# Performance work log

Hardware: AMD Instinct MI355X
Metric: run time of the kernel (lower is better)

Reference implementation:

```python
import jax, jax.numpy as jnp
import numpy as np

B, D_EMB, D_HID, D_FEAT = 16384, 128, 1024, 4096


def setup_inputs() -> dict:
    key = jax.random.key(0)
    ks = jax.random.split(key, 7)
    s = 0.05  # keep pre-sigmoid logits in a reasonable range
    return {
        "flat_emb": jax.random.normal(ks[0], (B, D_FEAT), dtype=jnp.float32),
        "fs1_ctx_bias": jax.random.normal(ks[1], (1, D_EMB), dtype=jnp.float32),
        "fs2_ctx_bias": jax.random.normal(ks[2], (1, D_EMB), dtype=jnp.float32),
        "fs1_W1": jax.random.normal(ks[3], (D_EMB, D_HID), dtype=jnp.float32) * s,
        "fs1_b1": jnp.zeros((D_HID,), dtype=jnp.float32),
        "fs1_W2": jax.random.normal(ks[4], (D_HID, D_FEAT), dtype=jnp.float32) * s,
        "fs1_b2": jnp.zeros((D_FEAT,), dtype=jnp.float32),
        "fs2_W1": jax.random.normal(ks[5], (D_EMB, D_HID), dtype=jnp.float32) * s,
        "fs2_b1": jnp.zeros((D_HID,), dtype=jnp.float32),
        "fs2_W2": jax.random.normal(ks[6], (D_HID, D_FEAT), dtype=jnp.float32) * s,
        "fs2_b2": jnpp_zeros((D_FEAT,)) if False else jnp.zeros((D_FEAT,), dtype=jnp.float32),
    }


def _gate(ctx_bias, W1, b1, W2, b2):
    # DNN: Linear -> ReLU -> Linear -> sigmoid. ctx_bias is [1, D_EMB];
    # the torch code repeats it over the batch, which is mathematically a
    # broadcast — compute the gate once and broadcast-multiply.
    h = jax.nn.relu(ctx_bias @ W1 + b1)            # [1, D_HID]
    return jax.nn.sigmoid(h @ W2 + b2) * 2.0        # [1, D_FEAT]


def reference(flat_emb, fs1_ctx_bias, fs2_ctx_bias,
              fs1_W1, fs1_b1, fs1_W2, fs1_b2,
              fs2_W1, fs2_b1, fs2_W2, fs2_b2):
    gt1 = _gate(fs1_ctx_bias, fs1_W1, fs1_b1, fs1_W2, fs1_b2)
    gt2 = _gate(fs2_ctx_bias, fs2_W1, fs2_b1, fs2_W2, fs2_b2)
    feature1 = flat_emb * gt1   # [B, D_FEAT]
    feature2 = flat_emb * gt2   # [B, D_FEAT]
    return (feature1, feature2)
```

## Files before the change

### kernel.cpp

```cpp
#include <hip/hip_runtime.h>
#include <math.h>

#define B_SZ   16384
#define D_EMB  128
#define D_HID  1024
#define D_FEAT 4096

__global__ __launch_bounds__(256) void gate_kernel(
    const float* __restrict__ ctx1, const float* __restrict__ ctx2,
    const float* __restrict__ W1a,  const float* __restrict__ b1a,
    const float* __restrict__ W2a,  const float* __restrict__ b2a,
    const float* __restrict__ W1b,  const float* __restrict__ b1b,
    const float* __restrict__ W2b,  const float* __restrict__ b2b,
    float* __restrict__ gates )
{
    const int blocks_per_gate = D_FEAT / 256;
    const int g   = blockIdx.x / blocks_per_gate;
    const int blk = blockIdx.x % blocks_per_gate;

    const float* ctx = (g == 0) ? ctx1 : ctx2;
    const float* W1  = (g == 0) ? W1a  : W1b;
    const float* b1  = (g == 0) ? b1a  : b1b;
    const float* W2  = (g == 0) ? W2a  : W2b;
    const float* b2  = (g == 0) ? b2a  : b2b;

    __shared__ float s_ctx[D_EMB];
    __shared__ float s_h[D_HID];

    const int t = threadIdx.x;
    if (t < D_EMB) s_ctx[t] = ctx[t];
    __syncthreads();

#pragma unroll
    for (int r = 0; r < D_HID / 256; ++r) {
        const int m = t + 256 * r;
        float acc = b1[m];
#pragma unroll 8
        for (int i = 0; i < D_EMB; ++i)
            acc = fmaf(s_ctx[i], W1[i * D_HID + m], acc);
        s_h[m] = acc > 0.0f ? acc : 0.0f;
    }
    __syncthreads();

    const int j = blk * 256 + t;
    float acc = b2[j];
#pragma unroll 8
    for (int k = 0; k < D_HID; ++k)
        acc = fmaf(s_h[k], W2[k * D_FEAT + j], acc);

    const float gval = 2.0f / (1.0f + expf(-acc));
    gates[g * D_FEAT + j] = gval;
}

__global__ __launch_bounds__(256) void mul_kernel(
    const float4* __restrict__ emb,
    const float4* __restrict__ gates,
    float4* __restrict__ out1,
    float4* __restrict__ out2)
{
    const int idx = blockIdx.x * blockDim.x + threadIdx.x;
    const int total = B_SZ * D_FEAT / 4;
    if (idx >= total) return;

    const int jg = idx & (D_FEAT / 4 - 1);

    const float4 e  = emb[idx];
    const float4 g1 = gates[jg];
    const float4 g2 = gates[D_FEAT / 4 + jg];

    float4 o1, o2;
    o1.x = e.x * g1.x; o1.y = e.y * g1.y; o1.z = e.z * g1.z; o1.w = e.w * g1.w;
    o2.x = e.x * g2.x; o2.y = e.y * g2.y; o2.z = e.z * g2.z; o2.w = e.w * g2.w;

    out1[idx] = o1;
    out2[idx] = o2;
}

extern "C" void kernel_launch(void* const* d_in, const int* in_sizes, int n_in,
                              void* d_out, int out_size, void* d_ws, size_t ws_size,
                              hipStream_t stream)
{
    const float* flat_emb = (const float*)d_in[0];
    const float* ctx1     = (const float*)d_in[1];
    const float* ctx2     = (const float*)d_in[2];
    const float* W1a      = (const float*)d_in[3];
    const float* b1a      = (const float*)d_in[4];
    const float* W2a      = (const float*)d_in[5];
    const float* b2a      = (const float*)d_in[6];
    const float* W1b      = (const float*)d_in[7];
    const float* b1b      = (const float*)d_in[8];
    const float* W2b      = (const float*)d_in[9];
    const float* b2b      = (const float*)d_in[10];

    float* out1  = (float*)d_out;
    float* out2  = (float*)d_out + (size_t)B_SZ * D_FEAT;
    float* gates = (float*)d_ws;

    gate_kernel<<<2 * (D_FEAT / 256), 256, 0, stream>>>(
        ctx1, ctx2, W1a, b1a, W2a, b2a, W1b, b1b, W2b, b2b, gates);

    const int total4 = B_SZ * D_FEAT / 4;
    mul_kernel<<<total4 / 256, 256, 0, stream>>>(
        (const float4*)flat_emb, (const float4*)gates,
        (float4*)out1, (float4*)out2);
}
```

Baseline: 813.3 us.

## Split gate MLP into two kernels with split-K, and make the multiply kernel grid-stride with nontemporal accesses

The hidden layer is now computed once per gate in its own small kernel. Before, each of the 32 gate blocks recomputed the full hidden vector. The second layer uses 256 blocks that split the K dimension 8 ways and reduce the partial sums in shared memory, which gives far more parallelism than the old 32-block launch. The multiply kernel now runs a fixed 2048-block grid in which each thread loops over rows, loads its gate values once, and uses nontemporal loads and stores for the streaming data. The cost is one extra kernel launch and a workspace round trip for the hidden vector.

```diff
diff --git a/kernel.cpp b/kernel.cpp
--- a/kernel.cpp
+++ b/kernel.cpp
@@ -6,74 +6,98 @@
 #define D_HID  1024
 #define D_FEAT 4096
 
-__global__ __launch_bounds__(256) void gate_kernel(
+typedef float f4 __attribute__((ext_vector_type(4)));
+
+__global__ __launch_bounds__(256) void h_kernel(
     const float* __restrict__ ctx1, const float* __restrict__ ctx2,
     const float* __restrict__ W1a,  const float* __restrict__ b1a,
-    const float* __restrict__ W2a,  const float* __restrict__ b2a,
     const float* __restrict__ W1b,  const float* __restrict__ b1b,
-    const float* __restrict__ W2b,  const float* __restrict__ b2b,
-    float* __restrict__ gates )
+    float* __restrict__ h )
 {
-    const int blocks_per_gate = D_FEAT / 256;
-    const int g   = blockIdx.x / blocks_per_gate;
-    const int blk = blockIdx.x % blocks_per_gate;
-
-    const float* ctx = (g == 0) ? ctx1 : ctx2;
-    const float* W1  = (g == 0) ? W1a  : W1b;
-    const float* b1  = (g == 0) ? b1a  : b1b;
-    const float* W2  = (g == 0) ? W2a  : W2b;
-    const float* b2  = (g == 0) ? b2a  : b2b;
+    const int g   = blockIdx.x >> 2;
+    const int blk = blockIdx.x & 3;
+    const float* ctx = g ? ctx2 : ctx1;
+    const float* W1  = g ? W1b  : W1a;
+    const float* b1  = g ? b1b  : b1a;
 
     __shared__ float s_ctx[D_EMB];
-    __shared__ float s_h[D_HID];
-
     const int t = threadIdx.x;
     if (t < D_EMB) s_ctx[t] = ctx[t];
     __syncthreads();
 
+    const int m = blk * 256 + t;
+    float acc = b1[m];
+#pragma unroll 8
+    for (int i = 0; i < D_EMB; ++i)
+        acc = fmaf(s_ctx[i], W1[i * D_HID + m], acc);
+    h[g * D_HID + m] = acc > 0.0f ? acc : 0.0f;
+}
+
+__global__ __launch_bounds__(256) void gate_kernel(
+    const float* __restrict__ W2a, const float* __restrict__ b2a,
+    const float* __restrict__ W2b, const float* __restrict__ b2b,
+    const float* __restrict__ h,
+    float* __restrict__ gates       )
+{
+    const int g   = blockIdx.x >> 7;
+    const int blk = blockIdx.x & 127;
+    const float* W2 = g ? W2b : W2a;
+    const float* b2 = g ? b2b : b2a;
+
+    __shared__ float s_h[D_HID];
+    __shared__ float s_part[256];
+
+    const int t = threadIdx.x;
 #pragma unroll
-    for (int r = 0; r < D_HID / 256; ++r) {
-        const int m = t + 256 * r;
-        float acc = b1[m];
-#pragma unroll 8
-        for (int i = 0; i < D_EMB; ++i)
-            acc = fmaf(s_ctx[i], W1[i * D_HID + m], acc);
-        s_h[m] = acc > 0.0f ? acc : 0.0f;
-    }
+    for (int r = 0; r < D_HID / 256; ++r)
+        s_h[t + 256 * r] = h[g * D_HID + t + 256 * r];
     __syncthreads();
 
-    const int j = blk * 256 + t;
-    float acc = b2[j];
+    const int tj = t & 31;
+    const int tk = t >> 5;
+    const int j  = blk * 32 + tj;
+
+    const float* w = W2 + (size_t)(tk * 128) * D_FEAT + j;
+    float p = 0.0f;
 #pragma unroll 8
-    for (int k = 0; k < D_HID; ++k)
-        acc = fmaf(s_h[k], W2[k * D_FEAT + j], acc);
+    for (int kk = 0; kk < 128; ++kk)
+        p = fmaf(s_h[tk * 128 + kk], w[(size_t)kk * D_FEAT], p);
 
-    const float gval = 2.0f / (1.0f + expf(-acc));
-    gates[g * D_FEAT + j] = gval;
+    s_part[tj * 8 + tk] = p;
+    __syncthreads();
+
+    if (t < 32) {
+        float a = b2[blk * 32 + t];
+#pragma unroll
+        for (int u = 0; u < 8; ++u) a += s_part[t * 8 + u];
+        gates[g * D_FEAT + blk * 32 + t] = 2.0f / (1.0f + expf(-a));
+    }
 }
 
 __global__ __launch_bounds__(256) void mul_kernel(
-    const float4* __restrict__ emb,
-    const float4* __restrict__ gates,
-    float4* __restrict__ out1,
-    float4* __restrict__ out2)
+    const f4* __restrict__ emb,
+    const f4* __restrict__ gates,
+    f4* __restrict__ out1,
+    f4* __restrict__ out2)
 {
-    const int idx = blockIdx.x * blockDim.x + threadIdx.x;
-    const int total = B_SZ * D_FEAT / 4;
-    if (idx >= total) return;
+    const int tid = blockIdx.x * 256 + threadIdx.x;
+    const int c   = tid & (D_FEAT / 4 - 1);
+    const int r0  = tid >> 10;
 
-    const int jg = idx & (D_FEAT / 4 - 1);
+    const f4 g1 = gates[c];
+    const f4 g2 = gates[D_FEAT / 4 + c];
 
-    const float4 e  = emb[idx];
-    const float4 g1 = gates[jg];
-    const float4 g2 = gates[D_FEAT / 4 + jg];
+    size_t idx = (size_t)r0 * (D_FEAT / 4) + c;
+    const size_t step = (size_t)512 * (D_FEAT / 4);
 
-    float4 o1, o2;
-    o1.x = e.x * g1.x; o1.y = e.y * g1.y; o1.z = e.z * g1.z; o1.w = e.w * g1.w;
-    o2.x = e.x * g2.x; o2.y = e.y * g2.y; o2.z = e.z * g2.z; o2.w = e.w * g2.w;
-
-    out1[idx] = o1;
-    out2[idx] = o2;
+#pragma unroll 4
+    for (int r = 0; r < B_SZ / 512; ++r, idx += step) {
+        f4 e  = __builtin_nontemporal_load(emb + idx);
+        f4 o1 = e * g1;
+        f4 o2 = e * g2;
+        __builtin_nontemporal_store(o1, out1 + idx);
+        __builtin_nontemporal_store(o2, out2 + idx);
+    }
 }
 
 extern "C" void kernel_launch(void* const* d_in, const int* in_sizes, int n_in,
@@ -95,12 +119,12 @@
     float* out1  = (float*)d_out;
     float* out2  = (float*)d_out + (size_t)B_SZ * D_FEAT;
     float* gates = (float*)d_ws;
+    float* h     = (float*)d_ws + 2 * D_FEAT;
 
-    gate_kernel<<<2 * (D_FEAT / 256), 256, 0, stream>>>(
-        ctx1, ctx2, W1a, b1a, W2a, b2a, W1b, b1b, W2b, b2b, gates);
+    h_kernel<<<8, 256, 0, stream>>>(ctx1, ctx2, W1a, b1a, W1b, b1b, h);
 
-    const int total4 = B_SZ * D_FEAT / 4;
-    mul_kernel<<<total4 / 256, 256, 0, stream>>>(
-        (const float4*)flat_emb, (const float4*)gates,
-        (float4*)out1, (float4*)out2);
+    gate_kernel<<<256, 256, 0, stream>>>(W2a, b2a, W2b, b2b, h, gates);
+
+    mul_kernel<<<2048, 256, 0, stream>>>(
+        (const f4*)flat_emb, (const f4*)gates, (f4*)out1, (f4*)out2);
 }
```

New measurement: 738.4 us. 1.1x faster.
